# Performance work log

Measured on AMD Instinct MI355X. Metric: run time of the kernel, lower is better.

Reference implementation:

```python
import jax, jax.numpy as jnp
import numpy as np

B, N, C = 4096, 49, 256       # windows, tokens-per-window (7*7), channels
H, HD = 8, 32                 # heads, head_dim
WIN = 7                       # window side
M = 64                        # mask_shape (num windows per image)
SCALE = HD ** -0.5


def _relative_position_index():
    coords = np.stack(np.meshgrid(np.arange(WIN), np.arange(WIN), indexing='ij'))
    flat = coords.reshape(2, -1)                      # [2, 49]
    rel = flat[:, :, None] - flat[:, None, :]         # [2, 49, 49]
    rel = rel.transpose(1, 2, 0).astype(np.int32)     # [49, 49, 2]
    rel[:, :, 0] += WIN - 1
    rel[:, :, 1] += WIN - 1
    rel[:, :, 0] *= 2 * WIN - 1
    return rel.sum(-1)                                # [49, 49], values in [0, 169)


def setup_inputs() -> dict:
    key = jax.random.key(0)
    k1, k2, k3, k4, k5 = jax.random.split(key, 5)
    hidden_states = jax.random.normal(k1, (B, N, C), dtype=jnp.float32)
    attention_mask = jax.random.normal(k2, (M, N, N), dtype=jnp.float32)
    qkv_w = jax.random.normal(k3, (3 * C, C), dtype=jnp.float32) * 0.02
    qkv_b = jax.random.normal(k4, (3 * C,), dtype=jnp.float32) * 0.02
    bias_table = jax.random.normal(k5, ((2 * WIN - 1) ** 2, H), dtype=jnp.float32) * 0.02
    rel_index = jnp.asarray(_relative_position_index())
    return {"hidden_states": hidden_states, "attention_mask": attention_mask,
            "qkv_w": qkv_w, "qkv_b": qkv_b, "bias_table": bias_table,
            "rel_index": rel_index}


def reference(hidden_states, attention_mask, qkv_w, qkv_b, bias_table, rel_index):
    b, n, c = hidden_states.shape
    qkv = hidden_states @ qkv_w.T + qkv_b            # [B, N, 3C]
    q, k, v = jnp.split(qkv, 3, axis=-1)
    to_heads = lambda x: x.reshape(b, n, H, HD).transpose(0, 2, 1, 3)  # [B,H,N,HD]
    q, k, v = to_heads(q), to_heads(k), to_heads(v)

    # relative position bias: gather table -> [N, N, H] -> [H, N, N]
    bias = bias_table[rel_index.reshape(-1)].reshape(n, n, H).transpose(2, 0, 1)

    # mask[j] is applied to window-batch index b where j = b mod M
    m = attention_mask.shape[0]
    full = bias[None, None] + attention_mask[None, :, None]   # [1, M, H, N, N]
    full = jnp.broadcast_to(full, (b // m, m, H, n, n)).reshape(b, H, n, n)

    scores = jnp.einsum('bhqd,bhkd->bhqk', q, k) * SCALE + full
    attn = jax.nn.softmax(scores, axis=-1)
    ctx = jnp.einsum('bhqk,bhkd->bhqd', attn, v)
    return ctx.transpose(0, 2, 1, 3).reshape(b, n, c)
```

## Files before the change

kernel.cpp:

```cpp
#include <hip/hip_runtime.h>
#include <hip/hip_bf16.h>
#include <stdint.h>

typedef unsigned short u16;
typedef __attribute__((ext_vector_type(8))) short bf16x8;
typedef __attribute__((ext_vector_type(8))) unsigned short u16x8;
typedef __attribute__((ext_vector_type(4))) float f32x4;

#define NTOK 49
#define CDIM 256
#define NHEAD 8
#define HDIM 32
#define MWIN 64
#define SCALE_F 0.17677669529663687f

static __device__ inline u16 f2b(float f) {
    union { float f; unsigned u; } v; v.f = f;
    unsigned r = v.u + 0x7fff + ((v.u >> 16) & 1);
    return (u16)(r >> 16);
}

__global__ __launch_bounds__(256) void conv_bf16(
    const float* __restrict__ src, u16* __restrict__ dst, int n8)
{
    int i = blockIdx.x * 256 + threadIdx.x;
    if (i < n8) {
        float4 a = ((const float4*)src)[2 * i];
        float4 b = ((const float4*)src)[2 * i + 1];
        u16x8 v;
        v[0] = f2b(a.x); v[1] = f2b(a.y); v[2] = f2b(a.z); v[3] = f2b(a.w);
        v[4] = f2b(b.x); v[5] = f2b(b.y); v[6] = f2b(b.z); v[7] = f2b(b.w);
        ((u16x8*)dst)[i] = v;
    }
}

__global__ __launch_bounds__(256) void build_comb(
    const float* __restrict__ bias_table,
    const float* __restrict__ mask,
    const int*   __restrict__ rel_index,
    float* __restrict__ comb)
{
    int idx = blockIdx.x * 256 + threadIdx.x;
    int j = idx & 63, i = (idx >> 6) & 63, h = (idx >> 12) & 7, m = idx >> 15;
    float v = -1e9f;
    if (i < NTOK && j < NTOK) {
        int rel = rel_index[i * NTOK + j];
        v = bias_table[rel * NHEAD + h] + mask[m * (NTOK * NTOK) + i * NTOK + j];
    }
    comb[idx] = v;
}

__global__ __launch_bounds__(256) void qkv_gemm(
    const u16*  __restrict__ A,
    const u16*  __restrict__ Wt,
    const float* __restrict__ bias,
    u16* __restrict__ Cout)
{
    __shared__ u16 As[128 * 72];
    __shared__ u16 Bs[128 * 72];

    const int t = threadIdx.x;
    const int bm = blockIdx.x, bn = blockIdx.y;
    const int wave = t >> 6, lane = t & 63;
    const int wm = wave >> 1, wn = wave & 1;
    const int lrow = lane & 15, quad = lane >> 4;

    f32x4 acc[4][4];
#pragma unroll
    for (int i = 0; i < 4; i++)
#pragma unroll
        for (int j = 0; j < 4; j++) acc[i][j] = (f32x4){0.f, 0.f, 0.f, 0.f};

    const int srow = t >> 3;
    const int part = t & 7;
    const u16* Ab = A  + (size_t)(bm * 128) * CDIM + part * 8;
    const u16* Bb = Wt + (size_t)(bn * 128) * CDIM + part * 8;

#pragma unroll
    for (int kt = 0; kt < 4; kt++) {
        if (kt) __syncthreads();
        const int k0 = kt * 64;
#pragma unroll
        for (int r = 0; r < 4; r++) {
            int row = r * 32 + srow;
            *(int4*)&As[row * 72 + part * 8] = *(const int4*)&Ab[(size_t)row * CDIM + k0];
            *(int4*)&Bs[row * 72 + part * 8] = *(const int4*)&Bb[(size_t)row * CDIM + k0];
        }
        __syncthreads();
#pragma unroll
        for (int kk = 0; kk < 2; kk++) {
            const int kb = kk * 32 + quad * 8;
            bf16x8 af[4], bfr[4];
#pragma unroll
            for (int tm = 0; tm < 4; tm++)
                af[tm] = *(const bf16x8*)&As[(wm * 64 + tm * 16 + lrow) * 72 + kb];
#pragma unroll
            for (int tn = 0; tn < 4; tn++)
                bfr[tn] = *(const bf16x8*)&Bs[(wn * 64 + tn * 16 + lrow) * 72 + kb];
#pragma unroll
            for (int tm = 0; tm < 4; tm++)
#pragma unroll
                for (int tn = 0; tn < 4; tn++)
                    acc[tm][tn] = __builtin_amdgcn_mfma_f32_16x16x32_bf16(
                        af[tm], bfr[tn], acc[tm][tn], 0, 0, 0);
        }
    }

#pragma unroll
    for (int tn = 0; tn < 4; tn++) {
        int gcol = bn * 128 + wn * 64 + tn * 16 + lrow;
        float bv = bias[gcol];
#pragma unroll
        for (int tm = 0; tm < 4; tm++) {
            int grow0 = bm * 128 + wm * 64 + tm * 16 + quad * 4;
#pragma unroll
            for (int r = 0; r < 4; r++)
                Cout[(size_t)(grow0 + r) * 768 + gcol] = f2b(acc[tm][tn][r] + bv);
        }
    }
}

__global__ __launch_bounds__(64) void win_attn(
    const u16*   __restrict__ qkv,
    const float* __restrict__ comb,
    float* __restrict__ out,
    int b0)
{
    __shared__ u16 smem[7424];
    u16* q    = smem;
    u16* kbuf = smem + 2560;
    u16* vT   = smem + 5120;
    u16* P    = smem;

    const int lane = threadIdx.x;
    const int wloc = blockIdx.x;
    const int h = blockIdx.y;
    const int bg = b0 + wloc;
    const size_t rbase = (size_t)wloc * NTOK * 768;
    const int qoff = h * HDIM, koff = 256 + h * HDIM, voff = 512 + h * HDIM;

    for (int c = lane; c < NTOK * 4; c += 64) {
        int tok = c >> 2, p = (c & 3) * 8;
        *(int4*)&q[tok * 40 + p]    = *(const int4*)&qkv[rbase + (size_t)tok * 768 + qoff + p];
        *(int4*)&kbuf[tok * 40 + p] = *(const int4*)&qkv[rbase + (size_t)tok * 768 + koff + p];
    }
    for (int c = lane; c < NTOK * HDIM; c += 64) {
        int tok = c >> 5, d = c & 31;
        vT[d * 72 + tok] = qkv[rbase + (size_t)tok * 768 + voff + d];
    }
    for (int c = lane; c < 15 * 40; c += 64) { q[NTOK * 40 + c] = 0; kbuf[NTOK * 40 + c] = 0; }
    for (int c = lane; c < 32 * 15; c += 64) { int d = c / 15; vT[d * 72 + NTOK + (c % 15)] = 0; }
    __syncthreads();

    const int lrow = lane & 15, quad = lane >> 4;

    f32x4 s[4][4];
#pragma unroll
    for (int i = 0; i < 4; i++)
#pragma unroll
        for (int j = 0; j < 4; j++) s[i][j] = (f32x4){0.f, 0.f, 0.f, 0.f};
    {
        const int kb = quad * 8;
        bf16x8 af[4], bfr[4];
#pragma unroll
        for (int tm = 0; tm < 4; tm++) af[tm]  = *(const bf16x8*)&q[(tm * 16 + lrow) * 40 + kb];
#pragma unroll
        for (int tn = 0; tn < 4; tn++) bfr[tn] = *(const bf16x8*)&kbuf[(tn * 16 + lrow) * 40 + kb];
#pragma unroll
        for (int tm = 0; tm < 4; tm++)
#pragma unroll
            for (int tn = 0; tn < 4; tn++)
                s[tm][tn] = __builtin_amdgcn_mfma_f32_16x16x32_bf16(af[tm], bfr[tn], s[tm][tn], 0, 0, 0);
    }

    const float* cb = comb + (((size_t)(bg & (MWIN - 1)) * NHEAD + h) << 12);
#pragma unroll
    for (int tm = 0; tm < 4; tm++)
#pragma unroll
        for (int r = 0; r < 4; r++) {
            int i = tm * 16 + quad * 4 + r;
            const float* crow = cb + i * 64 + lrow;
#pragma unroll
            for (int tn = 0; tn < 4; tn++)
                s[tm][tn][r] = s[tm][tn][r] * SCALE_F + crow[tn * 16];
        }

    __syncthreads();

#pragma unroll
    for (int tm = 0; tm < 4; tm++)
#pragma unroll
        for (int r = 0; r < 4; r++) {
            float mx = fmaxf(fmaxf(s[tm][0][r], s[tm][1][r]), fmaxf(s[tm][2][r], s[tm][3][r]));
            mx = fmaxf(mx, __shfl_xor(mx, 1));
            mx = fmaxf(mx, __shfl_xor(mx, 2));
            mx = fmaxf(mx, __shfl_xor(mx, 4));
            mx = fmaxf(mx, __shfl_xor(mx, 8));
            float e0 = __expf(s[tm][0][r] - mx);
            float e1 = __expf(s[tm][1][r] - mx);
            float e2 = __expf(s[tm][2][r] - mx);
            float e3 = __expf(s[tm][3][r] - mx);
            float sum = e0 + e1 + e2 + e3;
            sum += __shfl_xor(sum, 1);
            sum += __shfl_xor(sum, 2);
            sum += __shfl_xor(sum, 4);
            sum += __shfl_xor(sum, 8);
            float inv = 1.0f / sum;
            int i = tm * 16 + quad * 4 + r;
            P[i * 72 + lrow]      = f2b(e0 * inv);
            P[i * 72 + 16 + lrow] = f2b(e1 * inv);
            P[i * 72 + 32 + lrow] = f2b(e2 * inv);
            P[i * 72 + 48 + lrow] = f2b(e3 * inv);
        }
    __syncthreads();

    f32x4 o[4][2];
#pragma unroll
    for (int i = 0; i < 4; i++) { o[i][0] = (f32x4){0.f, 0.f, 0.f, 0.f}; o[i][1] = (f32x4){0.f, 0.f, 0.f, 0.f}; }
#pragma unroll
    for (int kk = 0; kk < 2; kk++) {
        const int kb = kk * 32 + quad * 8;
        bf16x8 pf[4], vf[2];
#pragma unroll
        for (int tm = 0; tm < 4; tm++) pf[tm] = *(const bf16x8*)&P[(tm * 16 + lrow) * 72 + kb];
#pragma unroll
        for (int tn = 0; tn < 2; tn++) vf[tn] = *(const bf16x8*)&vT[(tn * 16 + lrow) * 72 + kb];
#pragma unroll
        for (int tm = 0; tm < 4; tm++)
#pragma unroll
            for (int tn = 0; tn < 2; tn++)
                o[tm][tn] = __builtin_amdgcn_mfma_f32_16x16x32_bf16(pf[tm], vf[tn], o[tm][tn], 0, 0, 0);
    }

    float* ob = out + (size_t)bg * NTOK * CDIM + h * HDIM;
#pragma unroll
    for (int tm = 0; tm < 4; tm++)
#pragma unroll
        for (int r = 0; r < 4; r++) {
            int i = tm * 16 + quad * 4 + r;
            if (i < NTOK) {
#pragma unroll
                for (int tn = 0; tn < 2; tn++)
                    ob[(size_t)i * CDIM + tn * 16 + lrow] = o[tm][tn][r];
            }
        }
}

extern "C" void kernel_launch(void* const* d_in, const int* in_sizes, int n_in,
                              void* d_out, int out_size, void* d_ws, size_t ws_size,
                              hipStream_t stream) {
    const float* hidden     = (const float*)d_in[0];
    const float* mask       = (const float*)d_in[1];
    const float* qkv_w      = (const float*)d_in[2];
    const float* qkv_b      = (const float*)d_in[3];
    const float* bias_table = (const float*)d_in[4];
    const int*   rel_index  = (const int*)d_in[5];
    float* out = (float*)d_out;

    float* comb = (float*)d_ws;
    u16* wbuf = (u16*)((char*)d_ws + 8388608);
    int W = 1024;
    while (W > 128 && 8781824ull + (size_t)W * NTOK * 2048 > ws_size) W >>= 1;
    int nch = 4096 / W;
    u16* hbuf = wbuf + 196608;
    u16* qkvbuf = hbuf + (size_t)W * NTOK * CDIM;

    build_comb<<<dim3(2097152 / 256), dim3(256), 0, stream>>>(bias_table, mask, rel_index, comb);
    conv_bf16<<<dim3((196608 / 8 + 255) / 256), dim3(256), 0, stream>>>(qkv_w, wbuf, 196608 / 8);

    const int chunk_elems = W * NTOK * CDIM;
    for (int c = 0; c < nch; c++) {
        conv_bf16<<<dim3((chunk_elems / 8 + 255) / 256), dim3(256), 0, stream>>>(
            hidden + (size_t)c * chunk_elems, hbuf, chunk_elems / 8);
        qkv_gemm<<<dim3(W * NTOK / 128, 6), dim3(256), 0, stream>>>(
            hbuf, wbuf, qkv_b, qkvbuf);
        win_attn<<<dim3(W, NHEAD), dim3(64), 0, stream>>>(qkvbuf, comb, out, c * W);
    }
}
```

Before: 777.2 us.

## Reuse bias-mask tile across windows and stream GEMM tiles via direct-to-LDS loads

```diff
diff --git a/kernel.cpp b/kernel.cpp
--- a/kernel.cpp
+++ b/kernel.cpp
@@ -11,7 +11,6 @@
 #define CDIM 256
 #define NHEAD 8
 #define HDIM 32
-#define MWIN 64
 #define SCALE_F 0.17677669529663687f
 
 static __device__ inline u16 f2b(float f) {
@@ -19,6 +18,10 @@
     unsigned r = v.u + 0x7fff + ((v.u >> 16) & 1);
     return (u16)(r >> 16);
 }
+
+#define GLOAD_LDS16(g, l) __builtin_amdgcn_global_load_lds( \
+    (const __attribute__((address_space(1))) unsigned int*)(g), \
+    (__attribute__((address_space(3))) unsigned int*)(l), 16, 0, 0)
 
 __global__ __launch_bounds__(256) void conv_bf16(
     const float* __restrict__ src, u16* __restrict__ dst, int n8)
@@ -56,8 +59,8 @@
     const float* __restrict__ bias,
     u16* __restrict__ Cout)
 {
-    __shared__ u16 As[128 * 72];
-    __shared__ u16 Bs[128 * 72];
+    __shared__ u16 As[128 * 64];
+    __shared__ u16 Bs[128 * 64];
 
     const int t = threadIdx.x;
     const int bm = blockIdx.x, bn = blockIdx.y;
@@ -71,32 +74,32 @@
 #pragma unroll
         for (int j = 0; j < 4; j++) acc[i][j] = (f32x4){0.f, 0.f, 0.f, 0.f};
 
-    const int srow = t >> 3;
-    const int part = t & 7;
-    const u16* Ab = A  + (size_t)(bm * 128) * CDIM + part * 8;
-    const u16* Bb = Wt + (size_t)(bn * 128) * CDIM + part * 8;
+    const int dr = lane >> 3;
+    const int dc = ((lane & 7) ^ dr) * 8;
+    const u16* Ag = A  + (size_t)(bm * 128 + wave * 32) * CDIM;
+    const u16* Bg = Wt + (size_t)(bn * 128 + wave * 32) * CDIM;
 
 #pragma unroll
     for (int kt = 0; kt < 4; kt++) {
         if (kt) __syncthreads();
         const int k0 = kt * 64;
 #pragma unroll
-        for (int r = 0; r < 4; r++) {
-            int row = r * 32 + srow;
-            *(int4*)&As[row * 72 + part * 8] = *(const int4*)&Ab[(size_t)row * CDIM + k0];
-            *(int4*)&Bs[row * 72 + part * 8] = *(const int4*)&Bb[(size_t)row * CDIM + k0];
+        for (int i = 0; i < 4; i++) {
+            GLOAD_LDS16(Ag + (size_t)(i * 8 + dr) * CDIM + k0 + dc, &As[(wave * 32 + i * 8) * 64]);
+            GLOAD_LDS16(Bg + (size_t)(i * 8 + dr) * CDIM + k0 + dc, &Bs[(wave * 32 + i * 8) * 64]);
         }
         __syncthreads();
 #pragma unroll
         for (int kk = 0; kk < 2; kk++) {
-            const int kb = kk * 32 + quad * 8;
+            const int xr = kk * 4 + quad;
+            const int sw = ((xr ^ (lrow & 7)) << 3);
             bf16x8 af[4], bfr[4];
 #pragma unroll
             for (int tm = 0; tm < 4; tm++)
-                af[tm] = *(const bf16x8*)&As[(wm * 64 + tm * 16 + lrow) * 72 + kb];
+                af[tm] = *(const bf16x8*)&As[(wm * 64 + tm * 16 + lrow) * 64 + sw];
 #pragma unroll
             for (int tn = 0; tn < 4; tn++)
-                bfr[tn] = *(const bf16x8*)&Bs[(wn * 64 + tn * 16 + lrow) * 72 + kb];
+                bfr[tn] = *(const bf16x8*)&Bs[(wn * 64 + tn * 16 + lrow) * 64 + sw];
 #pragma unroll
             for (int tm = 0; tm < 4; tm++)
 #pragma unroll
@@ -120,130 +123,125 @@
     }
 }
 
-__global__ __launch_bounds__(64) void win_attn(
+__global__ __launch_bounds__(64, 2) void win_attn(
     const u16*   __restrict__ qkv,
     const float* __restrict__ comb,
     float* __restrict__ out,
-    int b0)
-{
-    __shared__ u16 smem[7424];
-    u16* q    = smem;
-    u16* kbuf = smem + 2560;
-    u16* vT   = smem + 5120;
-    u16* P    = smem;
-
-    const int lane = threadIdx.x;
-    const int wloc = blockIdx.x;
-    const int h = blockIdx.y;
-    const int bg = b0 + wloc;
-    const size_t rbase = (size_t)wloc * NTOK * 768;
-    const int qoff = h * HDIM, koff = 256 + h * HDIM, voff = 512 + h * HDIM;
-
-    for (int c = lane; c < NTOK * 4; c += 64) {
-        int tok = c >> 2, p = (c & 3) * 8;
-        *(int4*)&q[tok * 40 + p]    = *(const int4*)&qkv[rbase + (size_t)tok * 768 + qoff + p];
-        *(int4*)&kbuf[tok * 40 + p] = *(const int4*)&qkv[rbase + (size_t)tok * 768 + koff + p];
-    }
-    for (int c = lane; c < NTOK * HDIM; c += 64) {
-        int tok = c >> 5, d = c & 31;
-        vT[d * 72 + tok] = qkv[rbase + (size_t)tok * 768 + voff + d];
-    }
-    for (int c = lane; c < 15 * 40; c += 64) { q[NTOK * 40 + c] = 0; kbuf[NTOK * 40 + c] = 0; }
-    for (int c = lane; c < 32 * 15; c += 64) { int d = c / 15; vT[d * 72 + NTOK + (c % 15)] = 0; }
-    __syncthreads();
-
-    const int lrow = lane & 15, quad = lane >> 4;
-
-    f32x4 s[4][4];
-#pragma unroll
-    for (int i = 0; i < 4; i++)
-#pragma unroll
-        for (int j = 0; j < 4; j++) s[i][j] = (f32x4){0.f, 0.f, 0.f, 0.f};
-    {
-        const int kb = quad * 8;
+    int G4)
+{
+    __shared__ u16 vT[32 * 72];
+    __shared__ u16 P[64 * 72];
+
+    const int lane = threadIdx.x, lrow = lane & 15, quad = lane >> 4;
+    const int m = blockIdx.x;
+    const int h = blockIdx.y / G4;
+    const int grp = blockIdx.y % G4;
+    const int qo = h * HDIM, ko = CDIM + h * HDIM, vo = 2 * CDIM + h * HDIM;
+
+    f32x4 cmb[4][4];
+    const float* cb = comb + (((size_t)m * NHEAD + h) << 12);
+#pragma unroll
+    for (int tm = 0; tm < 4; tm++)
+#pragma unroll
+        for (int r = 0; r < 4; r++) {
+            const float* crow = cb + (tm * 16 + quad * 4 + r) * 64 + lrow;
+#pragma unroll
+            for (int tn = 0; tn < 4; tn++) cmb[tm][tn][r] = crow[tn * 16];
+        }
+
+    for (int c = lane; c < 32 * 15; c += 64) vT[(c / 15) * 72 + NTOK + (c % 15)] = 0;
+
+    for (int j = 0; j < 4; j++) {
+        const int lw = m + 64 * (grp * 4 + j);
+        const size_t rb = (size_t)lw * NTOK * 768;
+
+        for (int c = lane; c < NTOK * 8; c += 64) {
+            int tok = c >> 3, d0 = (c & 7) * 4;
+            uint2 v = *(const uint2*)&qkv[rb + (size_t)tok * 768 + vo + d0];
+            vT[(d0 + 0) * 72 + tok] = (u16)(v.x & 0xffff);
+            vT[(d0 + 1) * 72 + tok] = (u16)(v.x >> 16);
+            vT[(d0 + 2) * 72 + tok] = (u16)(v.y & 0xffff);
+            vT[(d0 + 3) * 72 + tok] = (u16)(v.y >> 16);
+        }
+
         bf16x8 af[4], bfr[4];
 #pragma unroll
-        for (int tm = 0; tm < 4; tm++) af[tm]  = *(const bf16x8*)&q[(tm * 16 + lrow) * 40 + kb];
-#pragma unroll
-        for (int tn = 0; tn < 4; tn++) bfr[tn] = *(const bf16x8*)&kbuf[(tn * 16 + lrow) * 40 + kb];
+        for (int tm = 0; tm < 4; tm++)
+            af[tm]  = *(const bf16x8*)&qkv[rb + (size_t)(tm * 16 + lrow) * 768 + qo + quad * 8];
+#pragma unroll
+        for (int tn = 0; tn < 4; tn++)
+            bfr[tn] = *(const bf16x8*)&qkv[rb + (size_t)(tn * 16 + lrow) * 768 + ko + quad * 8];
+
+        f32x4 s[4][4];
+#pragma unroll
+        for (int a = 0; a < 4; a++)
+#pragma unroll
+            for (int b = 0; b < 4; b++) s[a][b] = (f32x4){0.f, 0.f, 0.f, 0.f};
 #pragma unroll
         for (int tm = 0; tm < 4; tm++)
 #pragma unroll
             for (int tn = 0; tn < 4; tn++)
                 s[tm][tn] = __builtin_amdgcn_mfma_f32_16x16x32_bf16(af[tm], bfr[tn], s[tm][tn], 0, 0, 0);
-    }
-
-    const float* cb = comb + (((size_t)(bg & (MWIN - 1)) * NHEAD + h) << 12);
-#pragma unroll
-    for (int tm = 0; tm < 4; tm++)
-#pragma unroll
-        for (int r = 0; r < 4; r++) {
-            int i = tm * 16 + quad * 4 + r;
-            const float* crow = cb + i * 64 + lrow;
+
+#pragma unroll
+        for (int tm = 0; tm < 4; tm++)
 #pragma unroll
             for (int tn = 0; tn < 4; tn++)
-                s[tm][tn][r] = s[tm][tn][r] * SCALE_F + crow[tn * 16];
-        }
-
-    __syncthreads();
-
-#pragma unroll
-    for (int tm = 0; tm < 4; tm++)
-#pragma unroll
-        for (int r = 0; r < 4; r++) {
-            float mx = fmaxf(fmaxf(s[tm][0][r], s[tm][1][r]), fmaxf(s[tm][2][r], s[tm][3][r]));
-            mx = fmaxf(mx, __shfl_xor(mx, 1));
-            mx = fmaxf(mx, __shfl_xor(mx, 2));
-            mx = fmaxf(mx, __shfl_xor(mx, 4));
-            mx = fmaxf(mx, __shfl_xor(mx, 8));
-            float e0 = __expf(s[tm][0][r] - mx);
-            float e1 = __expf(s[tm][1][r] - mx);
-            float e2 = __expf(s[tm][2][r] - mx);
-            float e3 = __expf(s[tm][3][r] - mx);
-            float sum = e0 + e1 + e2 + e3;
-            sum += __shfl_xor(sum, 1);
-            sum += __shfl_xor(sum, 2);
-            sum += __shfl_xor(sum, 4);
-            sum += __shfl_xor(sum, 8);
-            float inv = 1.0f / sum;
-            int i = tm * 16 + quad * 4 + r;
-            P[i * 72 + lrow]      = f2b(e0 * inv);
-            P[i * 72 + 16 + lrow] = f2b(e1 * inv);
-            P[i * 72 + 32 + lrow] = f2b(e2 * inv);
-            P[i * 72 + 48 + lrow] = f2b(e3 * inv);
-        }
-    __syncthreads();
-
-    f32x4 o[4][2];
-#pragma unroll
-    for (int i = 0; i < 4; i++) { o[i][0] = (f32x4){0.f, 0.f, 0.f, 0.f}; o[i][1] = (f32x4){0.f, 0.f, 0.f, 0.f}; }
-#pragma unroll
-    for (int kk = 0; kk < 2; kk++) {
-        const int kb = kk * 32 + quad * 8;
-        bf16x8 pf[4], vf[2];
-#pragma unroll
-        for (int tm = 0; tm < 4; tm++) pf[tm] = *(const bf16x8*)&P[(tm * 16 + lrow) * 72 + kb];
-#pragma unroll
-        for (int tn = 0; tn < 2; tn++) vf[tn] = *(const bf16x8*)&vT[(tn * 16 + lrow) * 72 + kb];
-#pragma unroll
-        for (int tm = 0; tm < 4; tm++)
-#pragma unroll
-            for (int tn = 0; tn < 2; tn++)
-                o[tm][tn] = __builtin_amdgcn_mfma_f32_16x16x32_bf16(pf[tm], vf[tn], o[tm][tn], 0, 0, 0);
-    }
-
-    float* ob = out + (size_t)bg * NTOK * CDIM + h * HDIM;
-#pragma unroll
-    for (int tm = 0; tm < 4; tm++)
-#pragma unroll
-        for (int r = 0; r < 4; r++) {
-            int i = tm * 16 + quad * 4 + r;
-            if (i < NTOK) {
+#pragma unroll
+                for (int r = 0; r < 4; r++)
+                    s[tm][tn][r] = s[tm][tn][r] * SCALE_F + cmb[tm][tn][r];
+
+#pragma unroll
+        for (int tm = 0; tm < 4; tm++)
+#pragma unroll
+            for (int r = 0; r < 4; r++) {
+                float e0 = __expf(s[tm][0][r]);
+                float e1 = __expf(s[tm][1][r]);
+                float e2 = __expf(s[tm][2][r]);
+                float e3 = __expf(s[tm][3][r]);
+                float sum = e0 + e1 + e2 + e3;
+                sum += __shfl_xor(sum, 1);
+                sum += __shfl_xor(sum, 2);
+                sum += __shfl_xor(sum, 4);
+                sum += __shfl_xor(sum, 8);
+                float inv = 1.0f / sum;
+                int i = tm * 16 + quad * 4 + r;
+                P[i * 72 + lrow]      = f2b(e0 * inv);
+                P[i * 72 + 16 + lrow] = f2b(e1 * inv);
+                P[i * 72 + 32 + lrow] = f2b(e2 * inv);
+                P[i * 72 + 48 + lrow] = f2b(e3 * inv);
+            }
+
+        f32x4 o[4][2];
+#pragma unroll
+        for (int a = 0; a < 4; a++) { o[a][0] = (f32x4){0.f,0.f,0.f,0.f}; o[a][1] = (f32x4){0.f,0.f,0.f,0.f}; }
+#pragma unroll
+        for (int kk = 0; kk < 2; kk++) {
+            const int kb = kk * 32 + quad * 8;
+            bf16x8 pf[4], vf[2];
+#pragma unroll
+            for (int tm = 0; tm < 4; tm++) pf[tm] = *(const bf16x8*)&P[(tm * 16 + lrow) * 72 + kb];
+#pragma unroll
+            for (int tn = 0; tn < 2; tn++) vf[tn] = *(const bf16x8*)&vT[(tn * 16 + lrow) * 72 + kb];
+#pragma unroll
+            for (int tm = 0; tm < 4; tm++)
 #pragma unroll
                 for (int tn = 0; tn < 2; tn++)
-                    ob[(size_t)i * CDIM + tn * 16 + lrow] = o[tm][tn][r];
+                    o[tm][tn] = __builtin_amdgcn_mfma_f32_16x16x32_bf16(pf[tm], vf[tn], o[tm][tn], 0, 0, 0);
+        }
+
+        float* ob = out + (size_t)lw * NTOK * CDIM + h * HDIM;
+#pragma unroll
+        for (int tm = 0; tm < 4; tm++)
+#pragma unroll
+            for (int r = 0; r < 4; r++) {
+                int i = tm * 16 + quad * 4 + r;
+                if (i < NTOK) {
+                    ob[(size_t)i * CDIM + lrow]      = o[tm][0][r];
+                    ob[(size_t)i * CDIM + 16 + lrow] = o[tm][1][r];
+                }
             }
-        }
+    }
 }
 
 extern "C" void kernel_launch(void* const* d_in, const int* in_sizes, int n_in,
@@ -259,21 +257,26 @@
 
     float* comb = (float*)d_ws;
     u16* wbuf = (u16*)((char*)d_ws + 8388608);
-    int W = 1024;
-    while (W > 128 && 8781824ull + (size_t)W * NTOK * 2048 > ws_size) W >>= 1;
-    int nch = 4096 / W;
+    int W = 4096;
+    while (W > 256 &&
+           8388608ull + 393216ull + (size_t)W * NTOK * CDIM * 2
+                      + (size_t)W * NTOK * 768 * 2 + 65536ull > ws_size)
+        W >>= 1;
+    const int nch = 4096 / W;
+    const int G4 = W / 256;
     u16* hbuf = wbuf + 196608;
     u16* qkvbuf = hbuf + (size_t)W * NTOK * CDIM;
 
-    build_comb<<<dim3(2097152 / 256), dim3(256), 0, stream>>>(bias_table, mask, rel_index, comb);
-    conv_bf16<<<dim3((196608 / 8 + 255) / 256), dim3(256), 0, stream>>>(qkv_w, wbuf, 196608 / 8);
-
-    const int chunk_elems = W * NTOK * CDIM;
+    build_comb<<<dim3(8192), dim3(256), 0, stream>>>(bias_table, mask, rel_index, comb);
+    conv_bf16<<<dim3(96), dim3(256), 0, stream>>>(qkv_w, wbuf, 196608 / 8);
+
+    const int ce = W * NTOK * CDIM;
     for (int c = 0; c < nch; c++) {
-        conv_bf16<<<dim3((chunk_elems / 8 + 255) / 256), dim3(256), 0, stream>>>(
-            hidden + (size_t)c * chunk_elems, hbuf, chunk_elems / 8);
+        conv_bf16<<<dim3((ce / 8 + 255) / 256), dim3(256), 0, stream>>>(
+            hidden + (size_t)c * ce, hbuf, ce / 8);
         qkv_gemm<<<dim3(W * NTOK / 128, 6), dim3(256), 0, stream>>>(
             hbuf, wbuf, qkv_b, qkvbuf);
-        win_attn<<<dim3(W, NHEAD), dim3(64), 0, stream>>>(qkvbuf, comb, out, c * W);
-    }
-}
+        win_attn<<<dim3(64, NHEAD * G4), dim3(64), 0, stream>>>(
+            qkvbuf, comb, out + (size_t)c * ce, G4);
+    }
+}
```

After: 679.1 us. 12.6% less time.
